# Optimization experiments

Hardware: AMD Instinct MI355X
Metric: run time of the kernel (lower is better)

## Reference

```python
import jax, jax.numpy as jnp
import numpy as np

D_MODEL = 1024
BLOCK_SIZE = 2048


def setup_inputs() -> dict:
    key = jax.random.key(0)
    ks = jax.random.split(key, 9)
    B, T, C = 4, 2048, D_MODEL
    s = 1.0 / np.sqrt(C)
    return {
        "x": jax.random.normal(ks[0], (B, T, C), dtype=jnp.float32),
        "Wq": jax.random.normal(ks[1], (C, C), dtype=jnp.float32) * s,
        "bq": jnp.zeros((C,), dtype=jnp.float32),
        "Wk": jax.random.normal(ks[2], (C, C), dtype=jnp.float32) * s,
        "bk": jnp.zeros((C,), dtype=jnp.float32),
        "Wv": jax.random.normal(ks[3], (C, C), dtype=jnp.float32) * s,
        "bv": jnp.zeros((C,), dtype=jnp.float32),
        "Wo": jax.random.normal(ks[4], (C, C), dtype=jnp.float32) * s,
        "bo": jnp.zeros((C,), dtype=jnp.float32),
    }


def reference(x, Wq, bq, Wk, bk, Wv, bv, Wo, bo):
    B, T, C = x.shape
    q = x @ Wq + bq
    k = x @ Wk + bk
    v = x @ Wv + bv
    # NOTE: original module never splits heads; attention is over full d_model
    score = jnp.einsum("btc,bsc->bts", q, k) / jnp.sqrt(jnp.asarray(C, x.dtype))
    causal = jnp.tril(jnp.ones((T, T), dtype=bool))
    score = jnp.where(causal, score, jnp.asarray(-jnp.inf, x.dtype))
    probs = jax.nn.softmax(score, axis=-1)
    out = jnp.einsum("bts,bsc->btc", probs, v)
    return out @ Wo + bo
```

## Files before the change

### kernel.cpp

```cpp
#include <hip/hip_runtime.h>
#include <hip/hip_bf16.h>
#include <stdint.h>


typedef __attribute__((ext_vector_type(8))) __bf16 bf16x8;
typedef __attribute__((ext_vector_type(4))) float f32x4;

#define MFMA16(A, B, C) __builtin_amdgcn_mfma_f32_16x16x32_bf16(A, B, C, 0, 0, 0)
#define BAR() asm volatile("s_barrier" ::: "memory")

#define T_SEQ 2048
#define D_MOD 1024

static __device__ __forceinline__ void gload_lds16(const void* g, void* l) {
  __builtin_amdgcn_global_load_lds(
      (const __attribute__((address_space(1))) void*)g,
      (__attribute__((address_space(3))) void*)l, 16, 0, 0);
}

__global__ void cvt_bf16_kernel(const float* __restrict__ in,
                                __bf16* __restrict__ out, int n8) {
  int i = blockIdx.x * blockDim.x + threadIdx.x;
  if (i < n8) {
    const float4* p = (const float4*)(in + (size_t)i * 8);
    float4 a = p[0], b = p[1];
    bf16x8 o;
    o[0] = (__bf16)a.x; o[1] = (__bf16)a.y; o[2] = (__bf16)a.z; o[3] = (__bf16)a.w;
    o[4] = (__bf16)b.x; o[5] = (__bf16)b.y; o[6] = (__bf16)b.z; o[7] = (__bf16)b.w;
    *(bf16x8*)(out + (size_t)i * 8) = o;
  }
}

__global__ void transpose_cvt_kernel(const float* __restrict__ W,
                                     __bf16* __restrict__ Wt) {
  __shared__ float tile[32][33];
  int tx = threadIdx.x, ty = threadIdx.y;
  int bx = blockIdx.x * 32, by = blockIdx.y * 32;
#pragma unroll
  for (int i = 0; i < 4; i++)
    tile[ty + 8 * i][tx] = W[(size_t)(by + ty + 8 * i) * D_MOD + bx + tx];
  __syncthreads();
#pragma unroll
  for (int i = 0; i < 4; i++)
    Wt[(size_t)(bx + ty + 8 * i) * D_MOD + by + tx] = (__bf16)tile[tx][ty + 8 * i];
}

__global__ void transpose_v_kernel(const __bf16* __restrict__ V,
                                   __bf16* __restrict__ Vt) {
  __shared__ __bf16 tile[32][33];
  int tx = threadIdx.x, ty = threadIdx.y;
  int b = blockIdx.z;
  int t0 = blockIdx.x * 32, d0 = blockIdx.y * 32;
  const __bf16* Vb = V + (size_t)b * T_SEQ * D_MOD;
  __bf16* Vtb = Vt + (size_t)b * D_MOD * T_SEQ;
#pragma unroll
  for (int i = 0; i < 4; i++)
    tile[ty + 8 * i][tx] = Vb[(size_t)(t0 + ty + 8 * i) * D_MOD + d0 + tx];
  __syncthreads();
#pragma unroll
  for (int i = 0; i < 4; i++)
    Vtb[(size_t)(d0 + ty + 8 * i) * T_SEQ + t0 + tx] = tile[tx][ty + 8 * i];
}

template <int MODE>
__global__ __launch_bounds__(512, 2) void ugemm_kernel(
    const __bf16* __restrict__ A, const __bf16* __restrict__ Bt,
    const float* __restrict__ b0, const float* __restrict__ b1,
    const float* __restrict__ b2, void* __restrict__ o0,
    void* __restrict__ o1, void* __restrict__ o2, int lda, int ldb,
    size_t bsA, size_t bsB, size_t bsC) {
  __shared__ __align__(16) char lds[147456];
#define ABUF(p3) (lds + (p3) * 16384)
#define BBUF(p3) (lds + 49152 + (p3) * 32768)

  const int tid = threadIdx.x;
  const int w = tid >> 6, l = tid & 63;
  const int wr = w >> 2, wc = w & 3;
  const int z = blockIdx.z;

  int bm, bn, NT;
  if (MODE == 0) {
    const int cpx = gridDim.x >> 3;
    const int swz = ((int)blockIdx.x & 7) * cpx + ((int)blockIdx.x >> 3);
    bm = (swz / 12) * 128; bn = (swz % 12) * 256; NT = 16;
  } else if (MODE == 1) {
    const int cpx = gridDim.x >> 3;
    const int swz = ((int)blockIdx.x & 7) * cpx + ((int)blockIdx.x >> 3);
    bm = (swz >> 2) * 128; bn = (swz & 3) * 256; NT = 16;
  } else if (MODE == 2) {
    const int i = (int)blockIdx.x >> 2;
    bm = i * 128; bn = ((int)blockIdx.x & 3) * 256; NT = (i + 1) * 2;
  } else {
    const int i = blockIdx.x, j = blockIdx.y;
    if (2 * j > i) return;
    bm = i * 128; bn = j * 256; NT = 16;
  }
  A += (size_t)z * bsA;
  Bt += (size_t)z * bsB;

  const int grow = w * 16 + (l >> 2);
  const int cswz = (l & 3) ^ ((l >> 3) & 3);
  const int rlo = l & 15;
  const int xsw = (((l >> 4) ^ ((l >> 1) & 3)) << 4);

#define STAGE_A(t, p3)                                                       \
  {                                                                          \
    const __bf16* g = A + (size_t)(bm + grow) * lda + (t) * 64 + cswz * 8;   \
    char* d = ABUF(p3) + w * 1024 + l * 16;                                  \
    gload_lds16(g, d);                                                       \
    gload_lds16(g + 32, d + 8192);                                           \
  }
#define STAGE_B(t, p3)                                                       \
  {                                                                          \
    const __bf16* g = Bt + (size_t)(bn + grow) * ldb + (t) * 64 + cswz * 8;  \
    char* d = BBUF(p3) + w * 1024 + l * 16;                                  \
    gload_lds16(g, d);                                                       \
    gload_lds16(g + 32, d + 16384);                                          \
    const __bf16* g2 = g + (size_t)128 * ldb;                                \
    gload_lds16(g2, d + 8192);                                               \
    gload_lds16(g2 + 32, d + 8192 + 16384);                                  \
  }
#define LDA_FRAG(p3, i, kk)                                       \
  (*(const bf16x8*)(ABUF(p3) + (kk) * 8192 +                      \
                    (wr * 64 + (i) * 16 + rlo) * 64 + xsw))
#define LDB_FRAG(p3, n, kk)                                       \
  (*(const bf16x8*)(BBUF(p3) + (kk) * 16384 +                     \
                    (wc * 64 + (n) * 16 + rlo) * 64 + xsw))

  f32x4 acc[4][4] = {};
  STAGE_A(0, 0); STAGE_B(0, 0);
  STAGE_A(1, 1); STAGE_B(1, 1);
  asm volatile("s_waitcnt vmcnt(6)" ::: "memory");
  BAR();

  int p = 0, pn2 = 2;
  for (int t = 0; t < NT; ++t) {
    bf16x8 af[4][2], bf01[2][2], bf23[2][2];
#pragma unroll
    for (int i = 0; i < 4; i++) {
      af[i][0] = LDA_FRAG(p, i, 0);
      af[i][1] = LDA_FRAG(p, i, 1);
    }
#pragma unroll
    for (int n = 0; n < 2; n++) {
      bf01[n][0] = LDB_FRAG(p, n, 0);
      bf01[n][1] = LDB_FRAG(p, n, 1);
    }
    if (t + 2 < NT) STAGE_A(t + 2, pn2);
    BAR();
    __builtin_amdgcn_s_setprio(1);
#pragma unroll
    for (int i = 0; i < 4; i++)
#pragma unroll
      for (int n = 0; n < 2; n++) {
        acc[i][n] = MFMA16(af[i][0], bf01[n][0], acc[i][n]);
        acc[i][n] = MFMA16(af[i][1], bf01[n][1], acc[i][n]);
      }
    __builtin_amdgcn_s_setprio(0);
    BAR();
#pragma unroll
    for (int n = 0; n < 2; n++) {
      bf23[n][0] = LDB_FRAG(p, n + 2, 0);
      bf23[n][1] = LDB_FRAG(p, n + 2, 1);
    }
    if (t + 2 < NT) STAGE_B(t + 2, pn2);
    BAR();
    __builtin_amdgcn_s_setprio(1);
#pragma unroll
    for (int i = 0; i < 4; i++)
#pragma unroll
      for (int n = 0; n < 2; n++) {
        acc[i][n + 2] = MFMA16(af[i][0], bf23[n][0], acc[i][n + 2]);
        acc[i][n + 2] = MFMA16(af[i][1], bf23[n][1], acc[i][n + 2]);
      }
    __builtin_amdgcn_s_setprio(0);
    if (t + 2 < NT) {
      asm volatile("s_waitcnt vmcnt(6)" ::: "memory");
    } else {
      asm volatile("s_waitcnt vmcnt(0)" ::: "memory");
    }
    BAR();
    p = (p + 1 == 3) ? 0 : p + 1;
    pn2 = (pn2 + 1 == 3) ? 0 : pn2 + 1;
  }

  if (MODE == 0) {
    const int seg = bn >> 10;
    const float* bs = (seg == 0) ? b0 : (seg == 1) ? b1 : b2;
    __bf16* os = (__bf16*)((seg == 0) ? o0 : (seg == 1) ? o1 : o2);
    const int bnl = bn & 1023;
#pragma unroll
    for (int n = 0; n < 4; n++) {
      int col = bnl + wc * 64 + n * 16 + rlo;
      float bvv = bs[col];
#pragma unroll
      for (int m = 0; m < 4; m++) {
        int rowb = bm + wr * 64 + m * 16 + (l >> 4) * 4;
#pragma unroll
        for (int r = 0; r < 4; r++)
          os[(size_t)(rowb + r) * D_MOD + col] = (__bf16)(acc[m][n][r] + bvv);
      }
    }
  } else if (MODE == 1) {
    float* os = (float*)o0;
#pragma unroll
    for (int n = 0; n < 4; n++) {
      int col = bn + wc * 64 + n * 16 + rlo;
      float bvv = b0[col];
#pragma unroll
      for (int m = 0; m < 4; m++) {
        int rowb = bm + wr * 64 + m * 16 + (l >> 4) * 4;
#pragma unroll
        for (int r = 0; r < 4; r++)
          os[(size_t)(rowb + r) * D_MOD + col] = acc[m][n][r] + bvv;
      }
    }
  } else if (MODE == 2) {
    __bf16* os = (__bf16*)o0 + (size_t)z * bsC;
#pragma unroll
    for (int n = 0; n < 4; n++) {
      int col = bn + wc * 64 + n * 16 + rlo;
#pragma unroll
      for (int m = 0; m < 4; m++) {
        int rowb = bm + wr * 64 + m * 16 + (l >> 4) * 4;
#pragma unroll
        for (int r = 0; r < 4; r++)
          os[(size_t)(rowb + r) * D_MOD + col] = (__bf16)acc[m][n][r];
      }
    }
  } else {
    float* os = (float*)o0 + (size_t)z * bsC;
#pragma unroll
    for (int n = 0; n < 4; n++) {
      int col = bn + wc * 64 + n * 16 + rlo;
#pragma unroll
      for (int m = 0; m < 4; m++) {
        int rowb = bm + wr * 64 + m * 16 + (l >> 4) * 4;
#pragma unroll
        for (int r = 0; r < 4; r++) {
          int row = rowb + r;
          float v = acc[m][n][r] * 0.03125f;
          if (col > row) v = -1e30f;
          os[(size_t)row * T_SEQ + col] = v;
        }
      }
    }
  }
#undef ABUF
#undef BBUF
#undef STAGE_A
#undef STAGE_B
#undef LDA_FRAG
#undef LDB_FRAG
}

__global__ __launch_bounds__(256) void softmax_kernel(float* __restrict__ S,
                                                      size_t bstride) {
  const int t = blockIdx.x, b = blockIdx.y;
  float* Srow = S + (size_t)b * bstride + (size_t)t * T_SEQ;
  __bf16* Prow = (__bf16*)Srow;
  const int L = ((t + 1) + 127) & ~127;
  const int tid = threadIdx.x;
  const int base = tid * 8;
  const bool act = base < L;
  float v[8];
  float m = -1e30f;
  if (act) {
    float4 a = *(const float4*)(Srow + base);
    float4 c = *(const float4*)(Srow + base + 4);
    v[0] = a.x; v[1] = a.y; v[2] = a.z; v[3] = a.w;
    v[4] = c.x; v[5] = c.y; v[6] = c.z; v[7] = c.w;
#pragma unroll
    for (int j = 0; j < 8; j++) m = fmaxf(m, v[j]);
  }
#pragma unroll
  for (int off = 1; off < 64; off <<= 1) m = fmaxf(m, __shfl_xor(m, off));
  __shared__ float redm[4], reds[4];
  const int wave = tid >> 6, lane = tid & 63;
  if (lane == 0) redm[wave] = m;
  __syncthreads();
  m = fmaxf(fmaxf(redm[0], redm[1]), fmaxf(redm[2], redm[3]));
  float p[8];
  float s = 0.f;
  if (act) {
#pragma unroll
    for (int j = 0; j < 8; j++) {
      p[j] = __expf(v[j] - m);
      s += p[j];
    }
  }
#pragma unroll
  for (int off = 1; off < 64; off <<= 1) s += __shfl_xor(s, off);
  if (lane == 0) reds[wave] = s;
  __syncthreads();
  const float inv = 1.0f / (reds[0] + reds[1] + reds[2] + reds[3]);
  if (act) {
    bf16x8 o;
#pragma unroll
    for (int j = 0; j < 8; j++) o[j] = (__bf16)(p[j] * inv);
    *(bf16x8*)(Prow + base) = o;
  }
}

extern "C" void kernel_launch(void* const* d_in, const int* in_sizes, int n_in,
                              void* d_out, int out_size, void* d_ws,
                              size_t ws_size, hipStream_t stream) {
  const float* x = (const float*)d_in[0];
  const float* Wq = (const float*)d_in[1];
  const float* bq = (const float*)d_in[2];
  const float* Wk = (const float*)d_in[3];
  const float* bk = (const float*)d_in[4];
  const float* Wv = (const float*)d_in[5];
  const float* bv = (const float*)d_in[6];
  const float* Wo = (const float*)d_in[7];
  const float* bo = (const float*)d_in[8];

  char* ws = (char*)d_ws;
  const size_t MB = 1u << 20;
  const size_t TC = (size_t)T_SEQ * D_MOD;
  const size_t TT = (size_t)T_SEQ * T_SEQ;
  __bf16* xb    = (__bf16*)(ws);
  __bf16* Wqkvt = (__bf16*)(ws + 16 * MB);
  __bf16* Wot   = (__bf16*)(ws + 22 * MB);
  __bf16* Qb    = (__bf16*)(ws + 24 * MB);
  __bf16* Kb    = (__bf16*)(ws + 40 * MB);
  __bf16* Vb    = (__bf16*)(ws + 56 * MB);
  __bf16* Vtb   = (__bf16*)(ws);

  cvt_bf16_kernel<<<4096, 256, 0, stream>>>(x, xb, 8192 * D_MOD / 8);
  dim3 tb(32, 8);
  transpose_cvt_kernel<<<dim3(32, 32), tb, 0, stream>>>(Wq, Wqkvt);
  transpose_cvt_kernel<<<dim3(32, 32), tb, 0, stream>>>(Wk, Wqkvt + 1024 * 1024);
  transpose_cvt_kernel<<<dim3(32, 32), tb, 0, stream>>>(Wv, Wqkvt + 2048 * 1024);
  transpose_cvt_kernel<<<dim3(32, 32), tb, 0, stream>>>(Wo, Wot);
  ugemm_kernel<0><<<768, 512, 0, stream>>>(xb, Wqkvt, bq, bk, bv, Qb, Kb, Vb,
                                           D_MOD, D_MOD, 0, 0, 0);
  transpose_v_kernel<<<dim3(64, 32, 4), tb, 0, stream>>>(Vb, Vtb);

  const bool batched = ws_size >= 137 * MB;
  if (batched) {
    float* S = (float*)(ws + 72 * MB);
    __bf16* AO = Vb;
    ugemm_kernel<3><<<dim3(16, 8, 4), 512, 0, stream>>>(
        Qb, Kb, nullptr, nullptr, nullptr, S, nullptr, nullptr, D_MOD, D_MOD,
        TC, TC, TT);
    softmax_kernel<<<dim3(T_SEQ, 4), 256, 0, stream>>>(S, TT);
    ugemm_kernel<2><<<dim3(64, 1, 4), 512, 0, stream>>>(
        (const __bf16*)S, Vtb, nullptr, nullptr, nullptr, AO, nullptr, nullptr,
        2 * T_SEQ, T_SEQ, TT * 2, (size_t)D_MOD * T_SEQ, TC);
    ugemm_kernel<1><<<256, 512, 0, stream>>>(AO, Wot, bo, nullptr, nullptr,
                                             d_out, nullptr, nullptr, D_MOD,
                                             D_MOD, 0, 0, 0);
  } else {
    float* S = (float*)(ws + 56 * MB);
    __bf16* AO = Qb;
    for (int b = 0; b < 4; ++b) {
      ugemm_kernel<3><<<dim3(16, 8, 1), 512, 0, stream>>>(
          Qb + b * TC, Kb + b * TC, nullptr, nullptr, nullptr, S, nullptr,
          nullptr, D_MOD, D_MOD, 0, 0, 0);
      softmax_kernel<<<dim3(T_SEQ, 1), 256, 0, stream>>>(S, 0);
      ugemm_kernel<2><<<dim3(64, 1, 1), 512, 0, stream>>>(
          (const __bf16*)S, Vtb + b * TC, nullptr, nullptr, nullptr,
          AO + b * TC, nullptr, nullptr, 2 * T_SEQ, T_SEQ, 0, 0, 0);
    }
    ugemm_kernel<1><<<256, 512, 0, stream>>>(AO, Wot, bo, nullptr, nullptr,
                                             d_out, nullptr, nullptr, D_MOD,
                                             D_MOD, 0, 0, 0);
  }
}
```

Before: 201.0 us.

## Add 256x256-tile GEMM kernel for QKV projection and QK^T scores

Introduces a new gemm8 kernel with 256x256 output tiles per block (8x4 MFMA accumulators per wave), double-buffered LDS, and a four-quadrant MFMA schedule that interleaves fragment loads and global-to-LDS staging. It replaces the 128x256 kernel for the fused QKV projection and the causal score GEMM, halving the grid and skipping upper-triangle tiles at the coarser granularity. The aim is higher arithmetic intensity and less redundant operand traffic per FLOP, at the cost of more accumulator registers, more barriers per iteration, and fewer blocks, which can hurt occupancy and load balance. The old kernel is trimmed to only the PV and output-projection modes.

```diff
diff --git a/kernel.cpp b/kernel.cpp
--- a/kernel.cpp
+++ b/kernel.cpp
@@ -62,13 +62,197 @@
     Vtb[(size_t)(d0 + ty + 8 * i) * T_SEQ + t0 + tx] = tile[tx][ty + 8 * i];
 }
 
+template <int MG, int NG>
+static __device__ __forceinline__ void mfma_quad(f32x4 (&acc)[8][4],
+                                                 const bf16x8 (&aR)[4][2],
+                                                 const bf16x8 (&bR)[2][2]) {
+#pragma unroll
+  for (int i = 0; i < 4; i++)
+#pragma unroll
+    for (int n = 0; n < 2; n++)
+#pragma unroll
+      for (int kk = 0; kk < 2; kk++)
+        acc[MG * 4 + i][NG * 2 + n] =
+            MFMA16(aR[i][kk], bR[n][kk], acc[MG * 4 + i][NG * 2 + n]);
+}
+
 template <int MODE>
-__global__ __launch_bounds__(512, 2) void ugemm_kernel(
+__global__ __launch_bounds__(512, 2) void gemm8_kernel(
     const __bf16* __restrict__ A, const __bf16* __restrict__ Bt,
     const float* __restrict__ b0, const float* __restrict__ b1,
     const float* __restrict__ b2, void* __restrict__ o0,
     void* __restrict__ o1, void* __restrict__ o2, int lda, int ldb,
     size_t bsA, size_t bsB, size_t bsC) {
+  constexpr int NT = 16;
+  __shared__ __align__(16) char lds[131072];
+#define ABUF(p, h) (lds + ((p) * 2 + (h)) * 16384)
+#define BBUF(p, h) (lds + 65536 + ((p) * 2 + (h)) * 16384)
+
+  const int tid = threadIdx.x;
+  const int w = tid >> 6, l = tid & 63;
+  const int wr = w >> 2, wc = w & 3;
+  int bm, bn;
+  if (MODE == 0) {
+    const int cpx = gridDim.x >> 3;
+    const int swz = ((int)blockIdx.x & 7) * cpx + ((int)blockIdx.x >> 3);
+    bm = (swz / 12) * 256;
+    bn = (swz % 12) * 256;
+  } else {
+    if ((int)blockIdx.y > (int)blockIdx.x) return;
+    bm = blockIdx.x * 256;
+    bn = blockIdx.y * 256;
+  }
+  const int z = blockIdx.z;
+  A += (size_t)z * bsA;
+  Bt += (size_t)z * bsB;
+
+  const int grow = l >> 2;
+  const int cswz = (l & 3) ^ ((l >> 3) & 3);
+  const int rlo = l & 15;
+  const int xsw = (((l >> 4) ^ ((l >> 1) & 3)) << 4);
+
+#define STAGE_A(t, h)                                                        \
+  {                                                                          \
+    const __bf16* g = A + (size_t)(bm + (h) * 128 + w * 16 + grow) * lda +   \
+                      (t) * 64 + cswz * 8;                                   \
+    char* d = ABUF((t) & 1, h) + w * 1024 + l * 16;                          \
+    gload_lds16(g, d);                                                       \
+    gload_lds16(g + 32, d + 8192);                                           \
+  }
+#define STAGE_B(t, h)                                                        \
+  {                                                                          \
+    const __bf16* g = Bt + (size_t)(bn + (h) * 128 + w * 16 + grow) * ldb +  \
+                      (t) * 64 + cswz * 8;                                   \
+    char* d = BBUF((t) & 1, h) + w * 1024 + l * 16;                          \
+    gload_lds16(g, d);                                                       \
+    gload_lds16(g + 32, d + 8192);                                           \
+  }
+#define LDA_FRAG(p, g, i, kk)                                     \
+  (*(const bf16x8*)(ABUF(p, wr) + (kk) * 8192 +                   \
+                    ((g) * 64 + (i) * 16 + rlo) * 64 + xsw))
+#define LDB_FRAG(p, g, n, kk)                                     \
+  (*(const bf16x8*)(BBUF(p, (wc >> 1)) + (kk) * 8192 +            \
+                    ((wc & 1) * 64 + (g) * 32 + (n) * 16 + rlo) * 64 + xsw))
+
+  f32x4 acc[8][4] = {};
+  STAGE_A(0, 0); STAGE_A(0, 1);
+  STAGE_B(0, 0); STAGE_B(0, 1);
+  STAGE_A(1, 0); STAGE_A(1, 1);
+  asm volatile("s_waitcnt vmcnt(4)" ::: "memory");
+  BAR();
+
+  for (int t = 0; t < NT; ++t) {
+    const int p = t & 1;
+    bf16x8 a[4][2], b[2][2];
+#pragma unroll
+    for (int i = 0; i < 4; i++) {
+      a[i][0] = LDA_FRAG(p, 0, i, 0);
+      a[i][1] = LDA_FRAG(p, 0, i, 1);
+    }
+#pragma unroll
+    for (int n = 0; n < 2; n++) {
+      b[n][0] = LDB_FRAG(p, 0, n, 0);
+      b[n][1] = LDB_FRAG(p, 0, n, 1);
+    }
+    if (t + 1 < NT) STAGE_B(t + 1, 0);
+    BAR();
+    __builtin_amdgcn_s_setprio(1);
+    mfma_quad<0, 0>(acc, a, b);
+    __builtin_amdgcn_s_setprio(0);
+    BAR();
+    bf16x8 b2[2][2];
+#pragma unroll
+    for (int n = 0; n < 2; n++) {
+      b2[n][0] = LDB_FRAG(p, 1, n, 0);
+      b2[n][1] = LDB_FRAG(p, 1, n, 1);
+    }
+    if (t + 1 < NT) STAGE_B(t + 1, 1);
+    BAR();
+    __builtin_amdgcn_s_setprio(1);
+    mfma_quad<0, 1>(acc, a, b2);
+    __builtin_amdgcn_s_setprio(0);
+    BAR();
+#pragma unroll
+    for (int i = 0; i < 4; i++) {
+      a[i][0] = LDA_FRAG(p, 1, i, 0);
+      a[i][1] = LDA_FRAG(p, 1, i, 1);
+    }
+    BAR();
+    __builtin_amdgcn_s_setprio(1);
+    mfma_quad<1, 1>(acc, a, b2);
+    __builtin_amdgcn_s_setprio(0);
+    BAR();
+#pragma unroll
+    for (int n = 0; n < 2; n++) {
+      b[n][0] = LDB_FRAG(p, 0, n, 0);
+      b[n][1] = LDB_FRAG(p, 0, n, 1);
+    }
+    if (t + 2 < NT) {
+      STAGE_A(t + 2, 0); STAGE_A(t + 2, 1);
+      BAR();
+      __builtin_amdgcn_s_setprio(1);
+      mfma_quad<1, 0>(acc, a, b);
+      __builtin_amdgcn_s_setprio(0);
+      asm volatile("s_waitcnt vmcnt(4)" ::: "memory");
+      BAR();
+    } else {
+      BAR();
+      __builtin_amdgcn_s_setprio(1);
+      mfma_quad<1, 0>(acc, a, b);
+      __builtin_amdgcn_s_setprio(0);
+      asm volatile("s_waitcnt vmcnt(0)" ::: "memory");
+      BAR();
+    }
+  }
+
+  if (MODE == 0) {
+    const int seg = bn >> 10;
+    const float* bs = (seg == 0) ? b0 : (seg == 1) ? b1 : b2;
+    __bf16* os = (__bf16*)((seg == 0) ? o0 : (seg == 1) ? o1 : o2);
+    const int bnl = bn & 1023;
+#pragma unroll
+    for (int n4 = 0; n4 < 4; n4++) {
+      int col = bnl + wc * 64 + n4 * 16 + rlo;
+      float bvv = bs[col];
+#pragma unroll
+      for (int mi = 0; mi < 8; mi++) {
+        int row = bm + wr * 128 + mi * 16 + (l >> 4) * 4;
+#pragma unroll
+        for (int r = 0; r < 4; r++)
+          os[(size_t)(row + r) * D_MOD + col] = (__bf16)(acc[mi][n4][r] + bvv);
+      }
+    }
+  } else {
+    float* os = (float*)o0 + (size_t)z * bsC;
+#pragma unroll
+    for (int n4 = 0; n4 < 4; n4++) {
+      int col = bn + wc * 64 + n4 * 16 + rlo;
+#pragma unroll
+      for (int mi = 0; mi < 8; mi++) {
+        int rowb = bm + wr * 128 + mi * 16 + (l >> 4) * 4;
+#pragma unroll
+        for (int r = 0; r < 4; r++) {
+          int row = rowb + r;
+          float v = acc[mi][n4][r] * 0.03125f;
+          if (col > row) v = -1e30f;
+          os[(size_t)row * T_SEQ + col] = v;
+        }
+      }
+    }
+  }
+#undef ABUF
+#undef BBUF
+#undef STAGE_A
+#undef STAGE_B
+#undef LDA_FRAG
+#undef LDB_FRAG
+}
+
+template <int MODE>
+__global__ __launch_bounds__(512, 2) void ugemm_kernel(
+    const __bf16* __restrict__ A, const __bf16* __restrict__ Bt,
+    const float* __restrict__ b0, void* __restrict__ o0, int lda, int ldb,
+    size_t bsA, size_t bsB, size_t bsC) {
   __shared__ __align__(16) char lds[147456];
 #define ABUF(p3) (lds + (p3) * 16384)
 #define BBUF(p3) (lds + 49152 + (p3) * 32768)
@@ -79,21 +263,13 @@
   const int z = blockIdx.z;
 
   int bm, bn, NT;
-  if (MODE == 0) {
-    const int cpx = gridDim.x >> 3;
-    const int swz = ((int)blockIdx.x & 7) * cpx + ((int)blockIdx.x >> 3);
-    bm = (swz / 12) * 128; bn = (swz % 12) * 256; NT = 16;
-  } else if (MODE == 1) {
+  if (MODE == 1) {
     const int cpx = gridDim.x >> 3;
     const int swz = ((int)blockIdx.x & 7) * cpx + ((int)blockIdx.x >> 3);
     bm = (swz >> 2) * 128; bn = (swz & 3) * 256; NT = 16;
-  } else if (MODE == 2) {
+  } else {
     const int i = (int)blockIdx.x >> 2;
     bm = i * 128; bn = ((int)blockIdx.x & 3) * 256; NT = (i + 1) * 2;
-  } else {
-    const int i = blockIdx.x, j = blockIdx.y;
-    if (2 * j > i) return;
-    bm = i * 128; bn = j * 256; NT = 16;
   }
   A += (size_t)z * bsA;
   Bt += (size_t)z * bsB;
@@ -184,24 +360,7 @@
     pn2 = (pn2 + 1 == 3) ? 0 : pn2 + 1;
   }
 
-  if (MODE == 0) {
-    const int seg = bn >> 10;
-    const float* bs = (seg == 0) ? b0 : (seg == 1) ? b1 : b2;
-    __bf16* os = (__bf16*)((seg == 0) ? o0 : (seg == 1) ? o1 : o2);
-    const int bnl = bn & 1023;
-#pragma unroll
-    for (int n = 0; n < 4; n++) {
-      int col = bnl + wc * 64 + n * 16 + rlo;
-      float bvv = bs[col];
-#pragma unroll
-      for (int m = 0; m < 4; m++) {
-        int rowb = bm + wr * 64 + m * 16 + (l >> 4) * 4;
-#pragma unroll
-        for (int r = 0; r < 4; r++)
-          os[(size_t)(rowb + r) * D_MOD + col] = (__bf16)(acc[m][n][r] + bvv);
-      }
-    }
-  } else if (MODE == 1) {
+  if (MODE == 1) {
     float* os = (float*)o0;
 #pragma unroll
     for (int n = 0; n < 4; n++) {
@@ -215,7 +374,7 @@
           os[(size_t)(rowb + r) * D_MOD + col] = acc[m][n][r] + bvv;
       }
     }
-  } else if (MODE == 2) {
+  } else {
     __bf16* os = (__bf16*)o0 + (size_t)z * bsC;
 #pragma unroll
     for (int n = 0; n < 4; n++) {
@@ -226,23 +385,6 @@
 #pragma unroll
         for (int r = 0; r < 4; r++)
           os[(size_t)(rowb + r) * D_MOD + col] = (__bf16)acc[m][n][r];
-      }
-    }
-  } else {
-    float* os = (float*)o0 + (size_t)z * bsC;
-#pragma unroll
-    for (int n = 0; n < 4; n++) {
-      int col = bn + wc * 64 + n * 16 + rlo;
-#pragma unroll
-      for (int m = 0; m < 4; m++) {
-        int rowb = bm + wr * 64 + m * 16 + (l >> 4) * 4;
-#pragma unroll
-        for (int r = 0; r < 4; r++) {
-          int row = rowb + r;
-          float v = acc[m][n][r] * 0.03125f;
-          if (col > row) v = -1e30f;
-          os[(size_t)row * T_SEQ + col] = v;
-        }
       }
     }
   }
@@ -333,7 +475,7 @@
   transpose_cvt_kernel<<<dim3(32, 32), tb, 0, stream>>>(Wk, Wqkvt + 1024 * 1024);
   transpose_cvt_kernel<<<dim3(32, 32), tb, 0, stream>>>(Wv, Wqkvt + 2048 * 1024);
   transpose_cvt_kernel<<<dim3(32, 32), tb, 0, stream>>>(Wo, Wot);
-  ugemm_kernel<0><<<768, 512, 0, stream>>>(xb, Wqkvt, bq, bk, bv, Qb, Kb, Vb,
+  gemm8_kernel<0><<<384, 512, 0, stream>>>(xb, Wqkvt, bq, bk, bv, Qb, Kb, Vb,
                                            D_MOD, D_MOD, 0, 0, 0);
   transpose_v_kernel<<<dim3(64, 32, 4), tb, 0, stream>>>(Vb, Vtb);
 
@@ -341,30 +483,28 @@
   if (batched) {
     float* S = (float*)(ws + 72 * MB);
     __bf16* AO = Vb;
-    ugemm_kernel<3><<<dim3(16, 8, 4), 512, 0, stream>>>(
+    gemm8_kernel<3><<<dim3(8, 8, 4), 512, 0, stream>>>(
         Qb, Kb, nullptr, nullptr, nullptr, S, nullptr, nullptr, D_MOD, D_MOD,
         TC, TC, TT);
     softmax_kernel<<<dim3(T_SEQ, 4), 256, 0, stream>>>(S, TT);
     ugemm_kernel<2><<<dim3(64, 1, 4), 512, 0, stream>>>(
-        (const __bf16*)S, Vtb, nullptr, nullptr, nullptr, AO, nullptr, nullptr,
-        2 * T_SEQ, T_SEQ, TT * 2, (size_t)D_MOD * T_SEQ, TC);
-    ugemm_kernel<1><<<256, 512, 0, stream>>>(AO, Wot, bo, nullptr, nullptr,
-                                             d_out, nullptr, nullptr, D_MOD,
-                                             D_MOD, 0, 0, 0);
+        (const __bf16*)S, Vtb, nullptr, AO, 2 * T_SEQ, T_SEQ, TT * 2,
+        (size_t)D_MOD * T_SEQ, TC);
+    ugemm_kernel<1><<<256, 512, 0, stream>>>(AO, Wot, bo, d_out, D_MOD, D_MOD,
+                                             0, 0, 0);
   } else {
     float* S = (float*)(ws + 56 * MB);
     __bf16* AO = Qb;
     for (int b = 0; b < 4; ++b) {
-      ugemm_kernel<3><<<dim3(16, 8, 1), 512, 0, stream>>>(
+      gemm8_kernel<3><<<dim3(8, 8, 1), 512, 0, stream>>>(
           Qb + b * TC, Kb + b * TC, nullptr, nullptr, nullptr, S, nullptr,
           nullptr, D_MOD, D_MOD, 0, 0, 0);
       softmax_kernel<<<dim3(T_SEQ, 1), 256, 0, stream>>>(S, 0);
       ugemm_kernel<2><<<dim3(64, 1, 1), 512, 0, stream>>>(
-          (const __bf16*)S, Vtb + b * TC, nullptr, nullptr, nullptr,
-          AO + b * TC, nullptr, nullptr, 2 * T_SEQ, T_SEQ, 0, 0, 0);
-    }
-    ugemm_kernel<1><<<256, 512, 0, stream>>>(AO, Wot, bo, nullptr, nullptr,
-                                             d_out, nullptr, nullptr, D_MOD,
-                                             D_MOD, 0, 0, 0);
-  }
-}
+          (const __bf16*)S, Vtb + b * TC, nullptr, AO + b * TC, 2 * T_SEQ,
+          T_SEQ, 0, 0, 0);
+    }
+    ugemm_kernel<1><<<256, 512, 0, stream>>>(AO, Wot, bo, d_out, D_MOD, D_MOD,
+                                             0, 0, 0);
+  }
+}
```

Result: no change. 197.4 us (-1.8%).
